# Optimization experiments

Hardware: AMD Instinct MI355X
Metric: run time of the kernel (lower is better)

The kernel has to match this reference:

```python
import jax, jax.numpy as jnp
import numpy as np

B, L, H, E, R = 2, 512, 768, 512, 32768
H2 = H // 2


def setup_inputs() -> dict:
    key = jax.random.key(0)
    ks = jax.random.split(key, 16)
    s = 0.02
    inp = {
        "hidden_states": jax.random.normal(ks[0], (B, L, H), dtype=jnp.float32),
        "ent_start": jax.random.randint(ks[1], (B, E), 0, L, dtype=jnp.int32),
        "ent_label": jax.random.randint(ks[2], (B, E), 0, 3, dtype=jnp.int32),
        "rel_head": jax.random.randint(ks[3], (B, R), 0, E, dtype=jnp.int32),
        "rel_tail": jax.random.randint(ks[4], (B, R), 0, E, dtype=jnp.int32),
        "rel_label": jax.random.randint(ks[5], (B, R), 0, 2, dtype=jnp.int32),
        "entity_emb": jax.random.normal(ks[6], (3, H), dtype=jnp.float32) * s,
        "head_W1": jax.random.normal(ks[7], (2 * H, H), dtype=jnp.float32) * s,
        "head_b1": jnp.zeros((H,), dtype=jnp.float32),
        "head_W2": jax.random.normal(ks[8], (H, H2), dtype=jnp.float32) * s,
        "head_b2": jnp.zeros((H2,), dtype=jnp.float32),
        "tail_W1": jax.random.normal(ks[9], (2 * H, H), dtype=jnp.float32) * s,
        "tail_b1": jnp.zeros((H,), dtype=jnp.float32),
        "tail_W2": jax.random.normal(ks[10], (H, H2), dtype=jnp.float32) * s,
        "tail_b2": jnp.zeros((H2,), dtype=jnp.float32),
        "bil_W": jax.random.normal(ks[11], (2, H2, H2), dtype=jnp.float32) * s,
        "lin_W": jax.random.normal(ks[12], (2 * H2, 2), dtype=jnp.float32) * s,
        "lin_b": jnp.zeros((2,), dtype=jnp.float32),
    }
    return inp


def _mlp(x, W1, b1, W2, b2):
    # Linear -> ReLU -> (dropout=identity) -> Linear -> ReLU -> (dropout=identity)
    h = jax.nn.relu(jnp.einsum("brd,dh->brh", x, W1) + b1)
    return jax.nn.relu(jnp.einsum("brh,hk->brk", h, W2) + b2)


def reference(hidden_states, ent_start, ent_label, rel_head, rel_tail, rel_label,
              entity_emb, head_W1, head_b1, head_W2, head_b2,
              tail_W1, tail_b1, tail_W2, tail_b2, bil_W, lin_W, lin_b):
    # Gather entity start token index and label for each relation endpoint
    h_idx = jnp.take_along_axis(ent_start, rel_head, axis=1)  # [B,R]
    t_idx = jnp.take_along_axis(ent_start, rel_tail, axis=1)
    h_lab = jnp.take_along_axis(ent_label, rel_head, axis=1)
    t_lab = jnp.take_along_axis(ent_label, rel_tail, axis=1)

    # Gather hidden states at entity start positions: [B,R,H]
    h_tok = jnp.take_along_axis(hidden_states, h_idx[..., None], axis=1)
    t_tok = jnp.take_along_axis(hidden_states, t_idx[..., None], axis=1)

    head_repr = jnp.concatenate([h_tok, entity_emb[h_lab]], axis=-1)  # [B,R,2H]
    tail_repr = jnp.concatenate([t_tok, entity_emb[t_lab]], axis=-1)

    heads = _mlp(head_repr, head_W1, head_b1, head_W2, head_b2)  # [B,R,H2]
    tails = _mlp(tail_repr, tail_W1, tail_b1, tail_W2, tail_b2)

    # BiaffineAttention: bilinear(x1,x2) + linear(cat(x1,x2))
    bil = jnp.einsum("brd,ode,bre->bro", heads, bil_W, tails)  # [B,R,2]
    lin = jnp.einsum("brc,co->bro", jnp.concatenate([heads, tails], axis=-1), lin_W) + lin_b
    logits = bil + lin  # [B,R,2]

    # Per-doc mean cross-entropy, summed over docs (matches loss accumulation)
    logp = jax.nn.log_softmax(logits, axis=-1)
    ce = -jnp.take_along_axis(logp, rel_label[..., None], axis=-1)[..., 0]  # [B,R]
    loss = ce.mean(axis=-1).sum()

    return loss, logits.reshape(B * R, 2)
```

## Files before the change

### kernel.cpp

```cpp
#include <hip/hip_runtime.h>
#include <math.h>

#define BB 2
#define LL 512
#define HH 768
#define EE 512
#define RR 32768
#define H2 384
#define MM 1024

typedef __attribute__((ext_vector_type(8))) short     bf16x8;
typedef __attribute__((ext_vector_type(4))) float     f32x4;
typedef __attribute__((ext_vector_type(8))) unsigned short u16x8;

__device__ __forceinline__ unsigned short f2bf(float f) {
    unsigned int u = __float_as_uint(f);
    u = (u + 0x7FFFu + ((u >> 16) & 1u)) >> 16;
    return (unsigned short)u;
}

__global__ __launch_bounds__(256) void prep(
    const float* __restrict__ hW1, const float* __restrict__ tW1,
    const float* __restrict__ hW2, const float* __restrict__ tW2,
    const float* __restrict__ bilW,
    unsigned short* __restrict__ W1ht, unsigned short* __restrict__ W1tt,
    unsigned short* __restrict__ W2ht, unsigned short* __restrict__ W2tt,
    unsigned short* __restrict__ bW0t, unsigned short* __restrict__ bW1t,
    const float* __restrict__ hidden, const int* __restrict__ ent_start,
    const int* __restrict__ ent_label, const float* __restrict__ emb,
    unsigned short* __restrict__ Xbf)
{
    __shared__ unsigned short T[32 * 40];
    const int bid = blockIdx.x;
    const int t = threadIdx.x;

    if (bid >= 3168) {
        const int m = bid - 3168;
        if (t >= 192) return;
        const int b = m >> 9;
        const int idx = ent_start[m];
        const int lab = ent_label[m];
        float4 v0, v1;
        if (t < 96) {
            const float4* s = (const float4*)(hidden + (size_t)(b * LL + idx) * HH);
            v0 = s[2 * t]; v1 = s[2 * t + 1];
        } else {
            const float4* s = (const float4*)(emb + (size_t)lab * HH);
            v0 = s[2 * t - 192]; v1 = s[2 * t - 191];
        }
        u16x8 o;
        o[0] = f2bf(v0.x); o[1] = f2bf(v0.y); o[2] = f2bf(v0.z); o[3] = f2bf(v0.w);
        o[4] = f2bf(v1.x); o[5] = f2bf(v1.y); o[6] = f2bf(v1.z); o[7] = f2bf(v1.w);
        *(u16x8*)(Xbf + (size_t)m * 1536 + 8 * t) = o;
        return;
    }

    const float* src; unsigned short* dst; int K, N, tile;
    if (bid < 1152)      { src = hW1;            dst = W1ht; K = 1536; N = 768; tile = bid; }
    else if (bid < 2304) { src = tW1;            dst = W1tt; K = 1536; N = 768; tile = bid - 1152; }
    else if (bid < 2592) { src = hW2;            dst = W2ht; K = 768;  N = 384; tile = bid - 2304; }
    else if (bid < 2880) { src = tW2;            dst = W2tt; K = 768;  N = 384; tile = bid - 2592; }
    else if (bid < 3024) { src = bilW;           dst = bW0t; K = 384;  N = 384; tile = bid - 2880; }
    else                 { src = bilW + 384*384; dst = bW1t; K = 384;  N = 384; tile = bid - 3024; }
    const int tn = N >> 5;
    const int n0 = (tile % tn) * 32;
    const int k0 = (tile / tn) * 32;

    const int r  = t >> 3;
    const int c4 = (t & 7) * 4;
    const float4 g = *(const float4*)(src + (size_t)(k0 + r) * N + n0 + c4);
    T[(c4 + 0) * 40 + r] = f2bf(g.x);
    T[(c4 + 1) * 40 + r] = f2bf(g.y);
    T[(c4 + 2) * 40 + r] = f2bf(g.z);
    T[(c4 + 3) * 40 + r] = f2bf(g.w);
    __syncthreads();
    const int n  = t >> 3;
    const int k4 = (t & 7) * 4;
    *(ushort4*)(dst + (size_t)(n0 + n) * K + k0 + k4) = *(ushort4*)&T[n * 40 + k4];
}

template<bool RELU, bool BIAS, bool WF32, bool WBF16>
__global__ __launch_bounds__(256) void gemm_mfma(
    const unsigned short* __restrict__ A, int lda, int aoff1,
    const unsigned short* __restrict__ Bt0, const unsigned short* __restrict__ Bt1,
    int ldb, int bt_mrow, int Nh,
    const float* __restrict__ bias0, const float* __restrict__ bias1,
    int K, float* __restrict__ Cf, unsigned short* __restrict__ Cb, int ldc)
{
    __shared__ unsigned short As[64 * 40];
    __shared__ unsigned short Bs[64 * 40];

    const int tid = threadIdx.x;
    const int n0 = blockIdx.x * 64;
    const int m0 = blockIdx.y * 64;
    const int hf = (n0 >= Nh) ? 1 : 0;
    const unsigned short* Bt = hf ? Bt1 : Bt0;
    const int nc0 = n0 - (hf ? Nh : 0);
    const int aoff = hf ? aoff1 : 0;

    const int sr = tid >> 2;
    const int sk = (tid & 3) * 8;

    const unsigned short* Ap = A + (size_t)(m0 + sr) * lda + aoff + sk;
    const unsigned short* Bp = Bt + (size_t)((m0 >> 9) * bt_mrow + nc0 + sr) * ldb + sk;

    const int lane = tid & 63;
    const int wave = tid >> 6;
    const int wm = (wave & 1) * 32;
    const int wn = (wave >> 1) * 32;
    const int l15 = lane & 15;
    const int quad = lane >> 4;

    f32x4 acc00 = {}, acc01 = {}, acc10 = {}, acc11 = {};

    for (int k0 = 0; k0 < K; k0 += 32) {
        const u16x8 av = *(const u16x8*)(Ap + k0);
        const u16x8 bv = *(const u16x8*)(Bp + k0);
        __syncthreads();
        *(u16x8*)&As[sr * 40 + sk] = av;
        *(u16x8*)&Bs[sr * 40 + sk] = bv;
        __syncthreads();
        const bf16x8 a0 = *(const bf16x8*)&As[(wm + l15) * 40 + quad * 8];
        const bf16x8 a1 = *(const bf16x8*)&As[(wm + 16 + l15) * 40 + quad * 8];
        const bf16x8 b0 = *(const bf16x8*)&Bs[(wn + l15) * 40 + quad * 8];
        const bf16x8 b1 = *(const bf16x8*)&Bs[(wn + 16 + l15) * 40 + quad * 8];
        acc00 = __builtin_amdgcn_mfma_f32_16x16x32_bf16(a0, b0, acc00, 0, 0, 0);
        acc01 = __builtin_amdgcn_mfma_f32_16x16x32_bf16(a0, b1, acc01, 0, 0, 0);
        acc10 = __builtin_amdgcn_mfma_f32_16x16x32_bf16(a1, b0, acc10, 0, 0, 0);
        acc11 = __builtin_amdgcn_mfma_f32_16x16x32_bf16(a1, b1, acc11, 0, 0, 0);
    }

    float bias_v0 = 0.f, bias_v1 = 0.f;
    if (BIAS) {
        const float* bb = hf ? bias1 : bias0;
        bias_v0 = bb[nc0 + wn + l15];
        bias_v1 = bb[nc0 + wn + 16 + l15];
    }
    const f32x4 accs[2][2] = {{acc00, acc01}, {acc10, acc11}};
    #pragma unroll
    for (int mi = 0; mi < 2; ++mi) {
        #pragma unroll
        for (int ni = 0; ni < 2; ++ni) {
            const int col = n0 + wn + ni * 16 + l15;
            const float bv = ni ? bias_v1 : bias_v0;
            #pragma unroll
            for (int r = 0; r < 4; ++r) {
                const int row = m0 + wm + mi * 16 + quad * 4 + r;
                float v = accs[mi][ni][r];
                if (BIAS) v += bv;
                if (RELU) v = fmaxf(v, 0.f);
                if (WF32) Cf[(size_t)row * ldc + col] = v;
                if (WBF16) Cb[(size_t)row * ldc + col] = f2bf(v);
            }
        }
    }
}

__global__ __launch_bounds__(256) void lin_proj(
    const float* __restrict__ HT, const float* __restrict__ linW,
    float* __restrict__ hlin, float* __restrict__ tlin)
{
    const int tid = threadIdx.x;
    const int lane = tid & 63;
    const int wave = tid >> 6;
    const int m = blockIdx.x * 4 + wave;
    const float* hr = HT + (size_t)m * 768;
    const float* tr = hr + 384;
    float hl0 = 0.f, hl1 = 0.f, tl0 = 0.f, tl1 = 0.f;
    #pragma unroll
    for (int t = 0; t < 6; ++t) {
        const int c = lane + 64 * t;
        const float hv = hr[c];
        const float tv = tr[c];
        const float2 wh = *(const float2*)(linW + 2 * c);
        const float2 wt = *(const float2*)(linW + 2 * (384 + c));
        hl0 += hv * wh.x; hl1 += hv * wh.y;
        tl0 += tv * wt.x; tl1 += tv * wt.y;
    }
    #pragma unroll
    for (int o = 32; o >= 1; o >>= 1) {
        hl0 += __shfl_xor(hl0, o, 64);
        hl1 += __shfl_xor(hl1, o, 64);
        tl0 += __shfl_xor(tl0, o, 64);
        tl1 += __shfl_xor(tl1, o, 64);
    }
    if (lane == 0) {
        hlin[2 * m]     = hl0;
        hlin[2 * m + 1] = hl1;
        tlin[2 * m]     = tl0;
        tlin[2 * m + 1] = tl1;
    }
}

__global__ __launch_bounds__(256) void rel_gather(
    const float* __restrict__ Stab,
    const float* __restrict__ hlin, const float* __restrict__ tlin,
    const float* __restrict__ lin_b,
    const int* __restrict__ rel_head, const int* __restrict__ rel_tail,
    const int* __restrict__ rel_label,
    float* __restrict__ out, float* __restrict__ bsum)
{
    const int tid = threadIdx.x;
    const int i = blockIdx.x * 256 + tid;
    const int b = i >> 15;
    const int h = rel_head[i];
    const int t = rel_tail[i];
    const int lab = rel_label[i];
    const int mh = (b << 9) + h;
    const int mt = (b << 9) + t;

    const float2 hl = ((const float2*)hlin)[mh];
    const float2 tl = ((const float2*)tlin)[mt];
    const float* srow = Stab + (size_t)mh * 1024;
    const float z0 = srow[t]       + hl.x + tl.x + lin_b[0];
    const float z1 = srow[512 + t] + hl.y + tl.y + lin_b[1];
    out[1 + 2 * (size_t)i]     = z0;
    out[2 + 2 * (size_t)i]     = z1;

    const float mx = fmaxf(z0, z1);
    const float mn = fminf(z0, z1);
    const float lse = mx + log1pf(expf(mn - mx));
    float ce = lse - (lab ? z1 : z0);

    #pragma unroll
    for (int o = 32; o >= 1; o >>= 1) ce += __shfl_xor(ce, o, 64);
    __shared__ float wsum[4];
    if ((tid & 63) == 0) wsum[tid >> 6] = ce;
    __syncthreads();
    if (tid == 0) bsum[blockIdx.x] = wsum[0] + wsum[1] + wsum[2] + wsum[3];
}

__global__ __launch_bounds__(256) void finalize(
    const float* __restrict__ bsum, float* __restrict__ out)
{
    const int tid = threadIdx.x;
    float v = bsum[tid];
    #pragma unroll
    for (int o = 32; o >= 1; o >>= 1) v += __shfl_xor(v, o, 64);
    __shared__ float s[4];
    if ((tid & 63) == 0) s[tid >> 6] = v;
    __syncthreads();
    if (tid == 0) {
        out[0] = (s[0] + s[1] + s[2] + s[3]) * (1.0f / (float)RR);
    }
}

extern "C" void kernel_launch(void* const* d_in, const int* in_sizes, int n_in,
                              void* d_out, int out_size, void* d_ws, size_t ws_size,
                              hipStream_t stream) {
    const float* hidden    = (const float*)d_in[0];
    const int*   ent_start = (const int*)d_in[1];
    const int*   ent_label = (const int*)d_in[2];
    const int*   rel_head  = (const int*)d_in[3];
    const int*   rel_tail  = (const int*)d_in[4];
    const int*   rel_label = (const int*)d_in[5];
    const float* emb       = (const float*)d_in[6];
    const float* head_W1   = (const float*)d_in[7];
    const float* head_b1   = (const float*)d_in[8];
    const float* head_W2   = (const float*)d_in[9];
    const float* head_b2   = (const float*)d_in[10];
    const float* tail_W1   = (const float*)d_in[11];
    const float* tail_b1   = (const float*)d_in[12];
    const float* tail_W2   = (const float*)d_in[13];
    const float* tail_b2   = (const float*)d_in[14];
    const float* bil_W     = (const float*)d_in[15];
    const float* lin_W     = (const float*)d_in[16];
    const float* lin_b     = (const float*)d_in[17];
    float* out = (float*)d_out;

    char* w = (char*)d_ws;
    auto carve = [&](size_t bytes) {
        char* p = w; w += (bytes + 255) & ~(size_t)255; return p;
    };
    unsigned short* Xbf  = (unsigned short*)carve((size_t)MM * 1536 * 2);
    unsigned short* Y1bf = (unsigned short*)carve((size_t)MM * 1536 * 2);
    unsigned short* HTbf = (unsigned short*)carve((size_t)MM * 768 * 2);
    float*          HT   = (float*)carve((size_t)MM * 768 * 4);
    unsigned short* hWbf = (unsigned short*)carve((size_t)MM * 768 * 2);
    float*          Stab = (float*)carve((size_t)MM * 1024 * 4);
    unsigned short* W1ht = (unsigned short*)carve((size_t)768 * 1536 * 2);
    unsigned short* W1tt = (unsigned short*)carve((size_t)768 * 1536 * 2);
    unsigned short* W2ht = (unsigned short*)carve((size_t)384 * 768 * 2);
    unsigned short* W2tt = (unsigned short*)carve((size_t)384 * 768 * 2);
    unsigned short* bW0t = (unsigned short*)carve((size_t)384 * 384 * 2);
    unsigned short* bW1t = (unsigned short*)carve((size_t)384 * 384 * 2);
    float*          hlin = (float*)carve(2048 * 4);
    float*          tlin = (float*)carve(2048 * 4);
    float*          bsum = (float*)carve(256 * 4);

    prep<<<4192, 256, 0, stream>>>(
        head_W1, tail_W1, head_W2, tail_W2, bil_W,
        W1ht, W1tt, W2ht, W2tt, bW0t, bW1t,
        hidden, ent_start, ent_label, emb, Xbf);

    gemm_mfma<true, true, false, true><<<dim3(24, 16), 256, 0, stream>>>(
        Xbf, 1536, 0, W1ht, W1tt, 1536, 0, 768, head_b1, tail_b1, 1536,
        nullptr, Y1bf, 1536);

    gemm_mfma<true, true, true, true><<<dim3(12, 16), 256, 0, stream>>>(
        Y1bf, 1536, 768, W2ht, W2tt, 768, 0, 384, head_b2, tail_b2, 768,
        HT, HTbf, 768);

    gemm_mfma<false, false, false, true><<<dim3(12, 16), 256, 0, stream>>>(
        HTbf, 768, 0, bW0t, bW1t, 384, 0, 384, nullptr, nullptr, 384,
        nullptr, hWbf, 768);

    gemm_mfma<false, false, true, false><<<dim3(16, 16), 256, 0, stream>>>(
        hWbf, 768, 384, HTbf + 384, HTbf + 384, 768, 512, 512,
        nullptr, nullptr, 384, Stab, nullptr, 1024);

    lin_proj<<<256, 256, 0, stream>>>(HT, lin_W, hlin, tlin);

    rel_gather<<<256, 256, 0, stream>>>(Stab, hlin, tlin, lin_b,
                                        rel_head, rel_tail, rel_label, out, bsum);

    finalize<<<1, 256, 0, stream>>>(bsum, out);
}
```

Before: 161.5 us.

## Precompute label-embedding contribution to first MLP layer, halve GEMM K, prefetch tiles

The entity embedding half of the concatenated input only takes 3 distinct values, so its product with the lower half of W1 (plus bias) is precomputed once into a 3x1536 table. The first GEMM now runs with K=768 on the hidden tokens only and adds the table row chosen by each entity's label in its epilogue. This halves the W1 transpose work and the first GEMM's FLOPs. The change also adds register prefetch of the next K tile in the GEMM loop and interleaves the two bilinear outputs in Stab so the final gather can use a float2 load.

```diff
diff --git a/kernel.cpp b/kernel.cpp
--- a/kernel.cpp
+++ b/kernel.cpp
@@ -28,40 +28,67 @@
     unsigned short* __restrict__ bW0t, unsigned short* __restrict__ bW1t,
     const float* __restrict__ hidden, const int* __restrict__ ent_start,
     const int* __restrict__ ent_label, const float* __restrict__ emb,
-    unsigned short* __restrict__ Xbf)
+    const float* __restrict__ hb1, const float* __restrict__ tb1,
+    unsigned short* __restrict__ Hbf, float* __restrict__ embc)
 {
     __shared__ unsigned short T[32 * 40];
+    __shared__ float red[4][192];
     const int bid = blockIdx.x;
     const int t = threadIdx.x;
 
-    if (bid >= 3168) {
-        const int m = bid - 3168;
-        if (t >= 192) return;
+    if (bid >= 3040) {
+        const int eb = bid - 3040;
+        const int tc = t & 63;
+        const int kg = t >> 6;
+        const int n = eb * 64 + tc;
+        const float* W = (n < 768) ? hW1 : tW1;
+        const int cc = (n < 768) ? n : n - 768;
+        float a0 = 0.f, a1 = 0.f, a2 = 0.f;
+        const int kbeg = kg * 192;
+        #pragma unroll 8
+        for (int k = kbeg; k < kbeg + 192; ++k) {
+            const float w = W[(size_t)(768 + k) * 768 + cc];
+            a0 += emb[k] * w;
+            a1 += emb[768 + k] * w;
+            a2 += emb[1536 + k] * w;
+        }
+        red[kg][0 * 64 + tc] = a0;
+        red[kg][1 * 64 + tc] = a1;
+        red[kg][2 * 64 + tc] = a2;
+        __syncthreads();
+        if (kg == 0) {
+            const float b = (n < 768) ? hb1[n] : tb1[n - 768];
+            #pragma unroll
+            for (int l = 0; l < 3; ++l) {
+                embc[l * 1536 + n] = b + red[0][l * 64 + tc] + red[1][l * 64 + tc]
+                                       + red[2][l * 64 + tc] + red[3][l * 64 + tc];
+            }
+        }
+        return;
+    }
+
+    if (bid >= 2016) {
+        const int m = bid - 2016;
+        if (t >= 96) return;
         const int b = m >> 9;
         const int idx = ent_start[m];
-        const int lab = ent_label[m];
-        float4 v0, v1;
-        if (t < 96) {
-            const float4* s = (const float4*)(hidden + (size_t)(b * LL + idx) * HH);
-            v0 = s[2 * t]; v1 = s[2 * t + 1];
-        } else {
-            const float4* s = (const float4*)(emb + (size_t)lab * HH);
-            v0 = s[2 * t - 192]; v1 = s[2 * t - 191];
-        }
+        const float4* s = (const float4*)(hidden + (size_t)(b * LL + idx) * HH);
+        const float4 v0 = s[2 * t];
+        const float4 v1 = s[2 * t + 1];
         u16x8 o;
         o[0] = f2bf(v0.x); o[1] = f2bf(v0.y); o[2] = f2bf(v0.z); o[3] = f2bf(v0.w);
         o[4] = f2bf(v1.x); o[5] = f2bf(v1.y); o[6] = f2bf(v1.z); o[7] = f2bf(v1.w);
-        *(u16x8*)(Xbf + (size_t)m * 1536 + 8 * t) = o;
+        *(u16x8*)(Hbf + (size_t)m * 768 + 8 * t) = o;
         return;
     }
 
     const float* src; unsigned short* dst; int K, N, tile;
-    if (bid < 1152)      { src = hW1;            dst = W1ht; K = 1536; N = 768; tile = bid; }
-    else if (bid < 2304) { src = tW1;            dst = W1tt; K = 1536; N = 768; tile = bid - 1152; }
-    else if (bid < 2592) { src = hW2;            dst = W2ht; K = 768;  N = 384; tile = bid - 2304; }
-    else if (bid < 2880) { src = tW2;            dst = W2tt; K = 768;  N = 384; tile = bid - 2592; }
-    else if (bid < 3024) { src = bilW;           dst = bW0t; K = 384;  N = 384; tile = bid - 2880; }
-    else                 { src = bilW + 384*384; dst = bW1t; K = 384;  N = 384; tile = bid - 3024; }
+    if (bid < 576)       { src = hW1;            dst = W1ht; K = 768; N = 768; tile = bid; }
+    else if (bid < 1152) { src = tW1;            dst = W1tt; K = 768; N = 768; tile = bid - 576; }
+    else if (bid < 1440) { src = hW2;            dst = W2ht; K = 768; N = 384; tile = bid - 1152; }
+    else if (bid < 1728) { src = tW2;            dst = W2tt; K = 768; N = 384; tile = bid - 1440; }
+    else if (bid < 1872) { src = bilW;           dst = bW0t; K = 384; N = 384; tile = bid - 1728; }
+    else                 { src = bilW + 384*384; dst = bW1t; K = 384; N = 384; tile = bid - 1872; }
     const int tn = N >> 5;
     const int n0 = (tile % tn) * 32;
     const int k0 = (tile / tn) * 32;
@@ -79,12 +106,13 @@
     *(ushort4*)(dst + (size_t)(n0 + n) * K + k0 + k4) = *(ushort4*)&T[n * 40 + k4];
 }
 
-template<bool RELU, bool BIAS, bool WF32, bool WBF16>
+template<bool RELU, bool BIAS, bool EB, bool WF32, bool WBF16, bool O2>
 __global__ __launch_bounds__(256) void gemm_mfma(
     const unsigned short* __restrict__ A, int lda, int aoff1,
     const unsigned short* __restrict__ Bt0, const unsigned short* __restrict__ Bt1,
     int ldb, int bt_mrow, int Nh,
     const float* __restrict__ bias0, const float* __restrict__ bias1,
+    const float* __restrict__ embc, const int* __restrict__ labels,
     int K, float* __restrict__ Cf, unsigned short* __restrict__ Cb, int ldc)
 {
     __shared__ unsigned short As[64 * 40];
@@ -113,13 +141,18 @@
 
     f32x4 acc00 = {}, acc01 = {}, acc10 = {}, acc11 = {};
 
+    u16x8 av = *(const u16x8*)(Ap);
+    u16x8 bv = *(const u16x8*)(Bp);
+
     for (int k0 = 0; k0 < K; k0 += 32) {
-        const u16x8 av = *(const u16x8*)(Ap + k0);
-        const u16x8 bv = *(const u16x8*)(Bp + k0);
         __syncthreads();
         *(u16x8*)&As[sr * 40 + sk] = av;
         *(u16x8*)&Bs[sr * 40 + sk] = bv;
         __syncthreads();
+        if (k0 + 32 < K) {
+            av = *(const u16x8*)(Ap + k0 + 32);
+            bv = *(const u16x8*)(Bp + k0 + 32);
+        }
         const bf16x8 a0 = *(const bf16x8*)&As[(wm + l15) * 40 + quad * 8];
         const bf16x8 a1 = *(const bf16x8*)&As[(wm + 16 + l15) * 40 + quad * 8];
         const bf16x8 b0 = *(const bf16x8*)&Bs[(wn + l15) * 40 + quad * 8];
@@ -139,18 +172,27 @@
     const f32x4 accs[2][2] = {{acc00, acc01}, {acc10, acc11}};
     #pragma unroll
     for (int mi = 0; mi < 2; ++mi) {
+        int labr[4];
+        if (EB) {
+            #pragma unroll
+            for (int r = 0; r < 4; ++r)
+                labr[r] = labels[m0 + wm + mi * 16 + quad * 4 + r];
+        }
         #pragma unroll
         for (int ni = 0; ni < 2; ++ni) {
             const int col = n0 + wn + ni * 16 + l15;
             const float bv = ni ? bias_v1 : bias_v0;
+            int colw = col;
+            if (O2) colw = 2 * (nc0 + wn + ni * 16 + l15) + hf;
             #pragma unroll
             for (int r = 0; r < 4; ++r) {
                 const int row = m0 + wm + mi * 16 + quad * 4 + r;
                 float v = accs[mi][ni][r];
                 if (BIAS) v += bv;
+                if (EB) v += embc[labr[r] * 1536 + col];
                 if (RELU) v = fmaxf(v, 0.f);
-                if (WF32) Cf[(size_t)row * ldc + col] = v;
-                if (WBF16) Cb[(size_t)row * ldc + col] = f2bf(v);
+                if (WF32) Cf[(size_t)row * ldc + colw] = v;
+                if (WBF16) Cb[(size_t)row * ldc + colw] = f2bf(v);
             }
         }
     }
@@ -211,9 +253,9 @@
 
     const float2 hl = ((const float2*)hlin)[mh];
     const float2 tl = ((const float2*)tlin)[mt];
-    const float* srow = Stab + (size_t)mh * 1024;
-    const float z0 = srow[t]       + hl.x + tl.x + lin_b[0];
-    const float z1 = srow[512 + t] + hl.y + tl.y + lin_b[1];
+    const float2 zz = *(const float2*)(Stab + (size_t)mh * 1024 + 2 * t);
+    const float z0 = zz.x + hl.x + tl.x + lin_b[0];
+    const float z1 = zz.y + hl.y + tl.y + lin_b[1];
     out[1 + 2 * (size_t)i]     = z0;
     out[2 + 2 * (size_t)i]     = z1;
 
@@ -272,42 +314,43 @@
     auto carve = [&](size_t bytes) {
         char* p = w; w += (bytes + 255) & ~(size_t)255; return p;
     };
-    unsigned short* Xbf  = (unsigned short*)carve((size_t)MM * 1536 * 2);
+    unsigned short* Hbf  = (unsigned short*)carve((size_t)MM * 768 * 2);
     unsigned short* Y1bf = (unsigned short*)carve((size_t)MM * 1536 * 2);
     unsigned short* HTbf = (unsigned short*)carve((size_t)MM * 768 * 2);
     float*          HT   = (float*)carve((size_t)MM * 768 * 4);
     unsigned short* hWbf = (unsigned short*)carve((size_t)MM * 768 * 2);
     float*          Stab = (float*)carve((size_t)MM * 1024 * 4);
-    unsigned short* W1ht = (unsigned short*)carve((size_t)768 * 1536 * 2);
-    unsigned short* W1tt = (unsigned short*)carve((size_t)768 * 1536 * 2);
+    unsigned short* W1ht = (unsigned short*)carve((size_t)768 * 768 * 2);
+    unsigned short* W1tt = (unsigned short*)carve((size_t)768 * 768 * 2);
     unsigned short* W2ht = (unsigned short*)carve((size_t)384 * 768 * 2);
     unsigned short* W2tt = (unsigned short*)carve((size_t)384 * 768 * 2);
     unsigned short* bW0t = (unsigned short*)carve((size_t)384 * 384 * 2);
     unsigned short* bW1t = (unsigned short*)carve((size_t)384 * 384 * 2);
+    float*          embc = (float*)carve((size_t)3 * 1536 * 4);
     float*          hlin = (float*)carve(2048 * 4);
     float*          tlin = (float*)carve(2048 * 4);
     float*          bsum = (float*)carve(256 * 4);
 
-    prep<<<4192, 256, 0, stream>>>(
+    prep<<<3064, 256, 0, stream>>>(
         head_W1, tail_W1, head_W2, tail_W2, bil_W,
         W1ht, W1tt, W2ht, W2tt, bW0t, bW1t,
-        hidden, ent_start, ent_label, emb, Xbf);
-
-    gemm_mfma<true, true, false, true><<<dim3(24, 16), 256, 0, stream>>>(
-        Xbf, 1536, 0, W1ht, W1tt, 1536, 0, 768, head_b1, tail_b1, 1536,
-        nullptr, Y1bf, 1536);
-
-    gemm_mfma<true, true, true, true><<<dim3(12, 16), 256, 0, stream>>>(
-        Y1bf, 1536, 768, W2ht, W2tt, 768, 0, 384, head_b2, tail_b2, 768,
-        HT, HTbf, 768);
-
-    gemm_mfma<false, false, false, true><<<dim3(12, 16), 256, 0, stream>>>(
-        HTbf, 768, 0, bW0t, bW1t, 384, 0, 384, nullptr, nullptr, 384,
-        nullptr, hWbf, 768);
-
-    gemm_mfma<false, false, true, false><<<dim3(16, 16), 256, 0, stream>>>(
+        hidden, ent_start, ent_label, emb, head_b1, tail_b1, Hbf, embc);
+
+    gemm_mfma<true, false, true, false, true, false><<<dim3(24, 16), 256, 0, stream>>>(
+        Hbf, 768, 0, W1ht, W1tt, 768, 0, 768, nullptr, nullptr, embc, ent_label,
+        768, nullptr, Y1bf, 1536);
+
+    gemm_mfma<true, true, false, true, true, false><<<dim3(12, 16), 256, 0, stream>>>(
+        Y1bf, 1536, 768, W2ht, W2tt, 768, 0, 384, head_b2, tail_b2, nullptr, nullptr,
+        768, HT, HTbf, 768);
+
+    gemm_mfma<false, false, false, false, true, false><<<dim3(12, 16), 256, 0, stream>>>(
+        HTbf, 768, 0, bW0t, bW1t, 384, 0, 384, nullptr, nullptr, nullptr, nullptr,
+        384, nullptr, hWbf, 768);
+
+    gemm_mfma<false, false, false, true, false, true><<<dim3(16, 16), 256, 0, stream>>>(
         hWbf, 768, 384, HTbf + 384, HTbf + 384, 768, 512, 512,
-        nullptr, nullptr, 384, Stab, nullptr, 1024);
+        nullptr, nullptr, nullptr, nullptr, 384, Stab, nullptr, 1024);
 
     lin_proj<<<256, 256, 0, stream>>>(HT, lin_W, hlin, tlin);
 
```

Result: faster. 149.5 us (-7.4%).
